# Optimization experiments

Hardware: AMD Instinct MI355X
Metric: run time of the kernel (lower is better)

The kernel has to match this reference:

```python
import jax, jax.numpy as jnp
import numpy as np

B, N, C = 8192, 4, 1024
H = 16
D = C // H              # head_dim = 64
P = 4                   # proj_dim (Linformer reduced length)
IDX_I, IDX_J = 1, 2     # Return_attn_way(use_cls=True, attn_selet_way=0)
SCALE = D ** -0.5


def setup_inputs() -> dict:
    key = jax.random.key(0)
    ks = jax.random.split(key, 6)
    std = 0.02
    x = jax.random.normal(ks[0], (B, N, C), dtype=jnp.float32)
    W_qkv = jax.random.normal(ks[1], (C, 3 * C), dtype=jnp.float32) * std   # qkv_bias=False
    W_proj = jax.random.normal(ks[2], (C, C), dtype=jnp.float32) * std
    b_proj = jnp.zeros((C,), dtype=jnp.float32)
    W_E = jax.random.normal(ks[3], (P, N), dtype=jnp.float32) * std         # torch Linear weight [out,in]
    W_F = jax.random.normal(ks[4], (P, N), dtype=jnp.float32) * std
    return {"x": x, "W_qkv": W_qkv, "W_proj": W_proj, "b_proj": b_proj,
            "W_E": W_E, "W_F": W_F}


def reference(x, W_qkv, W_proj, b_proj, W_E, W_F):
    b, n, c = x.shape
    # qkv projection -> [B,N,3,H,D] -> q,k,v each [B,H,N,D]
    qkv = (x @ W_qkv).reshape(b, n, 3, H, D)
    qkv = jnp.transpose(qkv, (2, 0, 3, 1, 4))
    q, k, v = qkv[0], qkv[1], qkv[2]
    q = q * SCALE  # q_norm/k_norm are Identity (qk_norm=False)

    # gathered single-token score: q[:,:,IDX_I,:] @ k[:,:,IDX_J,:].T -> [B,H,H]
    # (torch transpose(-2,-1) on the [B,H,D] slice swaps H and D)
    attn_sel = jnp.einsum('bhd,bgd->bhg', q[:, :, IDX_I, :], k[:, :, IDX_J, :])
    attn_sel_sig = jax.nn.sigmoid(attn_sel)

    # Linformer E/F projection along the sequence axis: [B,H,N,D] -> [B,H,P,D]
    k_low = jnp.einsum('bhnd,pn->bhpd', k, W_E)
    v_low = jnp.einsum('bhnd,pn->bhpd', v, W_F)

    # reduced softmax attention: [B,H,N,P]
    attn = jnp.einsum('bhnd,bhpd->bhnp', q, k_low)
    attn = jax.nn.softmax(attn, axis=-1)  # attn_drop is identity (p=0, eval)
    out = jnp.einsum('bhnp,bhpd->bhnd', attn, v_low)

    # merge heads and output projection
    out = jnp.transpose(out, (0, 2, 1, 3)).reshape(b, n, c)
    out = out @ W_proj.T + b_proj  # proj_drop identity
    return (out, attn_sel_sig)
```

## Files before the change

kernel.cpp:

```cpp
#include <hip/hip_runtime.h>
#include <hip/hip_bf16.h>

#define B_   8192
#define C_   1024
#define H_   16
#define M_   (B_ * 4)
#define K_   1024
#define N1_  3072

typedef __attribute__((ext_vector_type(8))) short short8;
typedef __attribute__((ext_vector_type(4))) float f32x4;
typedef __attribute__((ext_vector_type(8))) int   int8v;

__device__ __forceinline__ unsigned short f2bf(float f) {
  union { float f; unsigned u; } v; v.f = f;
  unsigned r = v.u + 0x7fffu + ((v.u >> 16) & 1u);
  return (unsigned short)(r >> 16);
}
__device__ __forceinline__ float bf2f(unsigned short u) {
  union { unsigned u; float f; } v; v.u = ((unsigned)u) << 16;
  return v.f;
}
__device__ __forceinline__ int pk_fp8(float a, float b, float c, float d) {
  int r = __builtin_amdgcn_cvt_pk_fp8_f32(a, b, 0, false);
  r = __builtin_amdgcn_cvt_pk_fp8_f32(c, d, r, true);
  return r;
}

__device__ __forceinline__ size_t bpack(int j, int c) {
  return (size_t)(j >> 4) * 16384 + (size_t)(c >> 7) * 2048 +
         (size_t)((c >> 4) & 1) * 1024 + (size_t)((c >> 5) & 3) * 256 +
         (size_t)(j & 15) * 16 + (size_t)(c & 15);
}

__global__ __launch_bounds__(256) void cast_x_k(const float* __restrict__ x,
                                                unsigned char* __restrict__ x8,
                                                unsigned short* __restrict__ xsel) {
  const int row = blockIdx.x;
  const int tid = threadIdx.x;
  float4 v = ((const float4*)(x + (size_t)row * 1024))[tid];
  ((int*)(x8 + (size_t)row * 1024))[tid] = pk_fp8(v.x, v.y, v.z, v.w);
  const int n = row & 3;
  if (n == 1 || n == 2) {
    ushort4 o;
    o.x = f2bf(v.x); o.y = f2bf(v.y); o.z = f2bf(v.z); o.w = f2bf(v.w);
    ((ushort4*)(xsel + ((size_t)(n - 1) * 8192 + (row >> 2)) * 1024))[tid] = o;
  }
}

__global__ __launch_bounds__(256) void transpose_wqkv_k(const float* __restrict__ in,
                                                        unsigned short* __restrict__ outb,
                                                        unsigned char* __restrict__ out8) {
  __shared__ float t[32][33];
  int tx = threadIdx.x, ty = threadIdx.y;
  int j0 = blockIdx.x * 32, c0 = blockIdx.y * 32;
#pragma unroll
  for (int i = 0; i < 4; ++i)
    t[ty + i * 8][tx] = in[(size_t)(c0 + ty + i * 8) * N1_ + j0 + tx];
  __syncthreads();
#pragma unroll
  for (int i = 0; i < 4; ++i) {
    int j = j0 + ty + i * 8;
    int c = c0 + tx;
    float v = t[tx][ty + i * 8];
    if (j < 1024) v *= 0.125f;
    outb[(size_t)j * K_ + c] = f2bf(v);
    out8[bpack(j, c)] =
        (unsigned char)(__builtin_amdgcn_cvt_pk_fp8_f32(v * 32.f, v * 32.f, 0, false) & 0xff);
  }
}

__global__ __launch_bounds__(256) void cast_wproj_k(const float* __restrict__ in,
                                                    unsigned char* __restrict__ out) {
  int i = blockIdx.x * 256 + threadIdx.x;
  float4 v = ((const float4*)in)[i];
  int f = i * 4;
  int j = f >> 10, c = f & 1023;
  *(int*)(out + bpack(j, c)) = pk_fp8(v.x * 32.f, v.y * 32.f, v.z * 32.f, v.w * 32.f);
}

__global__ __launch_bounds__(256) void gemm_fixup(const unsigned short* __restrict__ A,
                                                  const unsigned short* __restrict__ B0,
                                                  unsigned short* __restrict__ Cbf) {
  __shared__ unsigned short lsA[128 * 32];
  __shared__ unsigned short lsB[128 * 32];
  const int K = 1024, Ncols = 1024;
  const int tid = threadIdx.x;
  const int wave = tid >> 6, lane = tid & 63;
  const int wm = (wave >> 1) * 64, wn = (wave & 1) * 64;
  const long tile_m = (long)blockIdx.y * 128, tile_n = (long)blockIdx.x * 128;
  const unsigned short* Bm = B0 + (tile_m >= 8192 ? (size_t)1024 * 1024 : 0);

  f32x4 acc[4][4] = {};
  const int ci0 = (wave * 2 + 0) * 64 + lane;
  const int ci1 = (wave * 2 + 1) * 64 + lane;
  const int r0 = ci0 >> 2, kc0 = (ci0 & 3) * 8;
  const int r1 = ci1 >> 2, kc1 = (ci1 & 3) * 8;
  const unsigned short* gA0 = A + (tile_m + r0) * K + kc0;
  const unsigned short* gA1 = A + (tile_m + r1) * K + kc1;
  const unsigned short* gB0 = Bm + (tile_n + r0) * K + kc0;
  const unsigned short* gB1 = Bm + (tile_n + r1) * K + kc1;
  unsigned short* dA0 = lsA + (wave * 2 + 0) * 512;
  unsigned short* dA1 = lsA + (wave * 2 + 1) * 512;
  unsigned short* dB0 = lsB + (wave * 2 + 0) * 512;
  unsigned short* dB1 = lsB + (wave * 2 + 1) * 512;
  const int r16 = lane & 15, q8 = (lane >> 4) * 8;

  for (int kt = 0; kt < K; kt += 32) {
    __builtin_amdgcn_global_load_lds((const __attribute__((address_space(1))) void*)(gA0 + kt),
                                     (__attribute__((address_space(3))) void*)dA0, 16, 0, 0);
    __builtin_amdgcn_global_load_lds((const __attribute__((address_space(1))) void*)(gA1 + kt),
                                     (__attribute__((address_space(3))) void*)dA1, 16, 0, 0);
    __builtin_amdgcn_global_load_lds((const __attribute__((address_space(1))) void*)(gB0 + kt),
                                     (__attribute__((address_space(3))) void*)dB0, 16, 0, 0);
    __builtin_amdgcn_global_load_lds((const __attribute__((address_space(1))) void*)(gB1 + kt),
                                     (__attribute__((address_space(3))) void*)dB1, 16, 0, 0);
    __syncthreads();
    short8 afr[4], bfr[4];
#pragma unroll
    for (int mi = 0; mi < 4; ++mi)
      afr[mi] = *(const short8*)&lsA[(wm + mi * 16 + r16) * 32 + q8];
#pragma unroll
    for (int ni = 0; ni < 4; ++ni)
      bfr[ni] = *(const short8*)&lsB[(wn + ni * 16 + r16) * 32 + q8];
#pragma unroll
    for (int mi = 0; mi < 4; ++mi)
#pragma unroll
      for (int ni = 0; ni < 4; ++ni)
        acc[mi][ni] = __builtin_amdgcn_mfma_f32_16x16x32_bf16(afr[mi], bfr[ni], acc[mi][ni], 0, 0, 0);
    __syncthreads();
  }
  const int cl = lane & 15, rq = (lane >> 4) * 4;
#pragma unroll
  for (int mi = 0; mi < 4; ++mi)
#pragma unroll
    for (int ni = 0; ni < 4; ++ni) {
      long col = tile_n + wn + ni * 16 + cl;
#pragma unroll
      for (int r = 0; r < 4; ++r) {
        long row = tile_m + wm + mi * 16 + rq + r;
        Cbf[(size_t)row * Ncols + col] = f2bf(acc[mi][ni][r]);
      }
    }
}

template <int OUTMODE>
__global__ __launch_bounds__(256) void gemm_mx(const unsigned char* __restrict__ A,
                                               const unsigned char* __restrict__ Bm,
                                               unsigned short* __restrict__ Cbf,
                                               float* __restrict__ Cf,
                                               const float* __restrict__ bias,
                                               int Ncols, int sA, int sB) {
  __shared__ unsigned char lds[49152];

  const int tid = threadIdx.x;
  const int wave = tid >> 6, lane = tid & 63;
  const int wm = (wave >> 1) * 64, wn = (wave & 1) * 64;
  const int tile_m = blockIdx.y * 128, tile_n = blockIdx.x * 128;

  f32x4 acc[4][4] = {};

  unsigned offA[4];
#pragma unroll
  for (int j = 0; j < 4; ++j) {
    int ci = j * 256 + tid;
    int qgs = ci >> 8, id = ci & 255;
    int r2 = (id >> 3) & 1, r3 = (id >> 4) & 1;
    int rr0 = ((id >> 1) & 1) ^ r2, rr1 = ((id >> 2) & 1) ^ r3;
    int row = rr0 | (rr1 << 1) | (r2 << 2) | (r3 << 3) | ((id >> 5) << 4);
    int half = (id & 1) ^ rr0;
    offA[j] = (unsigned)((tile_m + row) * K_ + qgs * 32 + half * 16);
  }

  const int hl = lane & 15, qg = lane >> 4;
  const int swz = (hl & 12) << 3;
  const int laneFragBase = qg * 4096 + ((hl * 32) ^ swz) + ((hl & 1) << 4);

  const unsigned char* gB = Bm + (size_t)((tile_n + wn) >> 4) * 16384 + (size_t)lane * 16;

  auto stageA = [&](int t) {
    unsigned char* dA = lds + (t % 3) * 16384;
    const int kt = t << 7;
#pragma unroll
    for (int j = 0; j < 4; ++j)
      __builtin_amdgcn_global_load_lds(
          (const __attribute__((address_space(1))) void*)(A + offA[j] + kt),
          (__attribute__((address_space(3))) void*)(dA + (j * 256 + wave * 64) * 16), 16, 0, 0);
  };

  int8v b[4];
  auto loadB = [&](int t) {
    const int kt16 = t * 2048;
#pragma unroll
    for (int ni = 0; ni < 4; ++ni) {
      const unsigned char* bp = gB + (size_t)ni * 16384 + kt16;
      int4 h0 = *(const int4*)bp;
      int4 h1 = *(const int4*)(bp + 1024);
      b[ni] = int8v{h0.x, h0.y, h0.z, h0.w, h1.x, h1.y, h1.z, h1.w};
    }
  };

  stageA(0);
  stageA(1);
  loadB(0);

#pragma unroll
  for (int t = 0; t < 8; ++t) {
    if (t < 7) asm volatile("s_waitcnt vmcnt(12)" ::: "memory");
    else       asm volatile("s_waitcnt vmcnt(8)" ::: "memory");
    __builtin_amdgcn_s_barrier();
    if (t + 2 < 8) stageA(t + 2);

    unsigned char* bA = lds + (t % 3) * 16384;
    __builtin_amdgcn_s_setprio(1);
#pragma unroll
    for (int mi = 0; mi < 4; ++mi) {
      int ad = (wm + mi * 16) * 32 + laneFragBase;
      int4 h0 = *(const int4*)(bA + ad);
      int4 h1 = *(const int4*)(bA + (ad ^ 16));
      int8v af = int8v{h0.x, h0.y, h0.z, h0.w, h1.x, h1.y, h1.z, h1.w};
#pragma unroll
      for (int ni = 0; ni < 4; ++ni)
        acc[mi][ni] = __builtin_amdgcn_mfma_scale_f32_16x16x128_f8f6f4(
            af, b[ni], acc[mi][ni], 0, 0, 0, sA, 0, sB);
    }
    __builtin_amdgcn_s_setprio(0);

    if (t + 1 < 8) loadB(t + 1);
  }

  const int cl = lane & 15, rq = (lane >> 4) * 4;
#pragma unroll
  for (int mi = 0; mi < 4; ++mi)
#pragma unroll
    for (int ni = 0; ni < 4; ++ni) {
      long col = tile_n + wn + ni * 16 + cl;
      float bv = (OUTMODE == 1) ? bias[col] : 0.f;
#pragma unroll
      for (int r = 0; r < 4; ++r) {
        long row = tile_m + wm + mi * 16 + rq + r;
        if (OUTMODE == 0)
          Cbf[(size_t)row * Ncols + col] = f2bf(acc[mi][ni][r]);
        else
          Cf[(size_t)row * Ncols + col] = acc[mi][ni][r] + bv;
      }
    }
}

__global__ __launch_bounds__(256) void attn_mfma_k(const unsigned short* __restrict__ qkv,
                                                   const unsigned short* __restrict__ q1,
                                                   const unsigned short* __restrict__ k2,
                                                   const float* __restrict__ WE,
                                                   const float* __restrict__ WF,
                                                   unsigned char* __restrict__ hmid8,
                                                   float* __restrict__ attn_sel) {
  __shared__ float As[4][16 * 17 + 2];
  const int tid = threadIdx.x;
  const int wave = tid >> 6, lane = tid & 63;
  const int b = blockIdx.x * 4 + wave;
  const size_t qb = (size_t)b * 4 * N1_;
  const int hl = lane & 15, qg = lane >> 4;

  f32x4 accS[4][4] = {};
  f32x4 accSel = {};
#pragma unroll
  for (int ch = 0; ch < 2; ++ch) {
    const int off = ch * 32 + qg * 8;
    short8 qf[4], kf[4];
#pragma unroll
    for (int n = 0; n < 4; ++n)
      qf[n] = *(const short8*)(qkv + qb + (size_t)n * N1_ + 0 + hl * 64 + off);
#pragma unroll
    for (int m = 0; m < 4; ++m)
      kf[m] = *(const short8*)(qkv + qb + (size_t)m * N1_ + 1024 + hl * 64 + off);
#pragma unroll
    for (int n = 0; n < 4; ++n)
#pragma unroll
      for (int m = 0; m < 4; ++m)
        accS[n][m] = __builtin_amdgcn_mfma_f32_16x16x32_bf16(qf[n], kf[m], accS[n][m], 0, 0, 0);
    short8 qs = *(const short8*)(q1 + (size_t)b * 1024 + hl * 64 + off);
    short8 ks = *(const short8*)(k2 + (size_t)b * 1024 + hl * 64 + off);
    accSel = __builtin_amdgcn_mfma_f32_16x16x32_bf16(qs, ks, accSel, 0, 0, 0);
  }

#pragma unroll
  for (int r = 0; r < 4; ++r)
    attn_sel[(size_t)b * 256 + (qg * 4 + r) * 16 + hl] = 1.f / (1.f + __expf(-accSel[r]));

  if ((hl >> 2) == qg) {
    const int h = hl, rr = h & 3;
    float Sm[4][4];
#pragma unroll
    for (int n = 0; n < 4; ++n)
#pragma unroll
      for (int m = 0; m < 4; ++m) Sm[n][m] = accS[n][m][rr];
#pragma unroll
    for (int n = 0; n < 4; ++n) {
      float lg[4];
#pragma unroll
      for (int p = 0; p < 4; ++p)
        lg[p] = Sm[n][0] * WE[p * 4] + Sm[n][1] * WE[p * 4 + 1] +
                Sm[n][2] * WE[p * 4 + 2] + Sm[n][3] * WE[p * 4 + 3];
      float mx = fmaxf(fmaxf(lg[0], lg[1]), fmaxf(lg[2], lg[3]));
      float e0 = __expf(lg[0] - mx), e1 = __expf(lg[1] - mx);
      float e2 = __expf(lg[2] - mx), e3 = __expf(lg[3] - mx);
      float inv = 1.f / (e0 + e1 + e2 + e3);
      e0 *= inv; e1 *= inv; e2 *= inv; e3 *= inv;
#pragma unroll
      for (int m = 0; m < 4; ++m)
        As[wave][h * 17 + n * 4 + m] =
            e0 * WF[0 * 4 + m] + e1 * WF[1 * 4 + m] + e2 * WF[2 * 4 + m] + e3 * WF[3 * 4 + m];
    }
  }
  __syncthreads();

  {
    const int h = lane & 15, dg = lane >> 4;
    float Ap[4][4];
#pragma unroll
    for (int n = 0; n < 4; ++n)
#pragma unroll
      for (int m = 0; m < 4; ++m) Ap[n][m] = As[wave][h * 17 + n * 4 + m];

    float outv[4][16] = {};
#pragma unroll
    for (int m = 0; m < 4; ++m) {
      const unsigned short* vp = qkv + qb + (size_t)m * N1_ + 2048 + h * 64 + dg * 16;
      short8 v0 = *(const short8*)(vp);
      short8 v1 = *(const short8*)(vp + 8);
      float vf[16];
#pragma unroll
      for (int j = 0; j < 8; ++j) {
        vf[j] = bf2f((unsigned short)v0[j]);
        vf[8 + j] = bf2f((unsigned short)v1[j]);
      }
#pragma unroll
      for (int n = 0; n < 4; ++n)
#pragma unroll
        for (int d = 0; d < 16; ++d) outv[n][d] += Ap[n][m] * vf[d];
    }
#pragma unroll
    for (int n = 0; n < 4; ++n) {
      int w0 = pk_fp8(outv[n][0] * 32.f, outv[n][1] * 32.f, outv[n][2] * 32.f, outv[n][3] * 32.f);
      int w1 = pk_fp8(outv[n][4] * 32.f, outv[n][5] * 32.f, outv[n][6] * 32.f, outv[n][7] * 32.f);
      int w2 = pk_fp8(outv[n][8] * 32.f, outv[n][9] * 32.f, outv[n][10] * 32.f, outv[n][11] * 32.f);
      int w3 = pk_fp8(outv[n][12] * 32.f, outv[n][13] * 32.f, outv[n][14] * 32.f, outv[n][15] * 32.f);
      *(int4*)(hmid8 + ((size_t)b * 4 + n) * 1024 + h * 64 + dg * 16) = make_int4(w0, w1, w2, w3);
    }
  }
}

extern "C" void kernel_launch(void* const* d_in, const int* in_sizes, int n_in,
                              void* d_out, int out_size, void* d_ws, size_t ws_size,
                              hipStream_t stream) {
  (void)in_sizes; (void)n_in; (void)out_size; (void)ws_size;
  const float* x      = (const float*)d_in[0];
  const float* W_qkv  = (const float*)d_in[1];
  const float* W_proj = (const float*)d_in[2];
  const float* b_proj = (const float*)d_in[3];
  const float* W_E    = (const float*)d_in[4];
  const float* W_F    = (const float*)d_in[5];

  float* out0 = (float*)d_out;
  float* out1 = out0 + (size_t)M_ * C_;

  char* ws = (char*)d_ws;
  unsigned short* xsel   = (unsigned short*)(ws);
  unsigned short* wqkvTb = (unsigned short*)(ws + 33554432);
  unsigned short* qkv_bf = (unsigned short*)(ws);
  unsigned char*  x8     = (unsigned char*)(ws + 201326592);
  unsigned char*  hmid8  = x8;
  unsigned char*  wqkvT8 = (unsigned char*)(ws + 234881024);
  unsigned char*  wproj8 = (unsigned char*)(ws + 238026752);
  unsigned short* q1k2   = (unsigned short*)(ws + 239075328);

  cast_x_k<<<32768, 256, 0, stream>>>(x, x8, xsel);
  transpose_wqkv_k<<<dim3(96, 32), dim3(32, 8), 0, stream>>>(W_qkv, wqkvTb, wqkvT8);
  cast_wproj_k<<<1024, 256, 0, stream>>>(W_proj, wproj8);

  gemm_fixup<<<dim3(8, 128), 256, 0, stream>>>(xsel, wqkvTb, q1k2);

  gemm_mx<0><<<dim3(24, 256), 256, 0, stream>>>(x8, wqkvT8, qkv_bf, nullptr, nullptr,
                                                3072, 127, 122);

  attn_mfma_k<<<B_ / 4, 256, 0, stream>>>(qkv_bf, q1k2, q1k2 + (size_t)8192 * 1024,
                                          W_E, W_F, hmid8, out1);

  gemm_mx<1><<<dim3(8, 256), 256, 0, stream>>>(hmid8, wproj8, nullptr, out0, b_proj,
                                               1024, 122, 122);
}
```

Measured before the change: 546.7 us.

## Pre-pack A operands into MFMA fragment layout and drop LDS staging

The x cast kernel and the attention kernel now write their fp8 outputs directly in the pre-swizzled fragment layout already used for the B operand. The fp8 GEMM can then load A fragments straight from global memory into registers, with double-buffered register prefetch replacing the three-stage LDS pipeline and its barriers. This removes LDS traffic and synchronisation. In exchange, each wave loads its A fragments itself with no sharing through LDS, which raises global and L2 traffic and register pressure.

```diff
diff --git a/kernel.cpp b/kernel.cpp
--- a/kernel.cpp
+++ b/kernel.cpp
@@ -36,15 +36,41 @@
 __global__ __launch_bounds__(256) void cast_x_k(const float* __restrict__ x,
                                                 unsigned char* __restrict__ x8,
                                                 unsigned short* __restrict__ xsel) {
-  const int row = blockIdx.x;
-  const int tid = threadIdx.x;
-  float4 v = ((const float4*)(x + (size_t)row * 1024))[tid];
-  ((int*)(x8 + (size_t)row * 1024))[tid] = pk_fp8(v.x, v.y, v.z, v.w);
+  const int rg = blockIdx.x;
+  const int t = threadIdx.x;
+  const int hl = t >> 4;
+  const int ck = t & 15;
+  const int row = rg * 16 + hl;
   const int n = row & 3;
-  if (n == 1 || n == 2) {
-    ushort4 o;
-    o.x = f2bf(v.x); o.y = f2bf(v.y); o.z = f2bf(v.z); o.w = f2bf(v.w);
-    ((ushort4*)(xsel + ((size_t)(n - 1) * 8192 + (row >> 2)) * 1024))[tid] = o;
+  const float* xr = x + (size_t)row * 1024;
+  unsigned char* og = x8 + (size_t)rg * 16384 + hl * 16;
+  unsigned short* xr2 = (n == 1 || n == 2)
+      ? xsel + ((size_t)(n - 1) * 8192 + (row >> 2)) * 1024 : nullptr;
+#pragma unroll
+  for (int i = 0; i < 4; ++i) {
+    const int kk = ck + i * 16;
+    const int c = kk * 16;
+    float4 v0 = *(const float4*)(xr + c);
+    float4 v1 = *(const float4*)(xr + c + 4);
+    float4 v2 = *(const float4*)(xr + c + 8);
+    float4 v3 = *(const float4*)(xr + c + 12);
+    int4 o;
+    o.x = pk_fp8(v0.x, v0.y, v0.z, v0.w);
+    o.y = pk_fp8(v1.x, v1.y, v1.z, v1.w);
+    o.z = pk_fp8(v2.x, v2.y, v2.z, v2.w);
+    o.w = pk_fp8(v3.x, v3.y, v3.z, v3.w);
+    *(int4*)(og + (kk >> 3) * 2048 + (kk & 1) * 1024 + ((kk >> 1) & 3) * 256) = o;
+    if (xr2) {
+      ushort4 s0, s1, s2, s3;
+      s0.x = f2bf(v0.x); s0.y = f2bf(v0.y); s0.z = f2bf(v0.z); s0.w = f2bf(v0.w);
+      s1.x = f2bf(v1.x); s1.y = f2bf(v1.y); s1.z = f2bf(v1.z); s1.w = f2bf(v1.w);
+      s2.x = f2bf(v2.x); s2.y = f2bf(v2.y); s2.z = f2bf(v2.z); s2.w = f2bf(v2.w);
+      s3.x = f2bf(v3.x); s3.y = f2bf(v3.y); s3.z = f2bf(v3.z); s3.w = f2bf(v3.w);
+      *(ushort4*)(xr2 + c) = s0;
+      *(ushort4*)(xr2 + c + 4) = s1;
+      *(ushort4*)(xr2 + c + 8) = s2;
+      *(ushort4*)(xr2 + c + 12) = s3;
+    }
   }
 }
 
@@ -151,82 +177,45 @@
                                                float* __restrict__ Cf,
                                                const float* __restrict__ bias,
                                                int Ncols, int sA, int sB) {
-  __shared__ unsigned char lds[49152];
-
   const int tid = threadIdx.x;
   const int wave = tid >> 6, lane = tid & 63;
   const int wm = (wave >> 1) * 64, wn = (wave & 1) * 64;
   const int tile_m = blockIdx.y * 128, tile_n = blockIdx.x * 128;
 
   f32x4 acc[4][4] = {};
-
-  unsigned offA[4];
-#pragma unroll
-  for (int j = 0; j < 4; ++j) {
-    int ci = j * 256 + tid;
-    int qgs = ci >> 8, id = ci & 255;
-    int r2 = (id >> 3) & 1, r3 = (id >> 4) & 1;
-    int rr0 = ((id >> 1) & 1) ^ r2, rr1 = ((id >> 2) & 1) ^ r3;
-    int row = rr0 | (rr1 << 1) | (r2 << 2) | (r3 << 3) | ((id >> 5) << 4);
-    int half = (id & 1) ^ rr0;
-    offA[j] = (unsigned)((tile_m + row) * K_ + qgs * 32 + half * 16);
-  }
-
-  const int hl = lane & 15, qg = lane >> 4;
-  const int swz = (hl & 12) << 3;
-  const int laneFragBase = qg * 4096 + ((hl * 32) ^ swz) + ((hl & 1) << 4);
-
+  const unsigned char* gA = A + (size_t)((tile_m + wm) >> 4) * 16384 + (size_t)lane * 16;
   const unsigned char* gB = Bm + (size_t)((tile_n + wn) >> 4) * 16384 + (size_t)lane * 16;
 
-  auto stageA = [&](int t) {
-    unsigned char* dA = lds + (t % 3) * 16384;
-    const int kt = t << 7;
-#pragma unroll
-    for (int j = 0; j < 4; ++j)
-      __builtin_amdgcn_global_load_lds(
-          (const __attribute__((address_space(1))) void*)(A + offA[j] + kt),
-          (__attribute__((address_space(3))) void*)(dA + (j * 256 + wave * 64) * 16), 16, 0, 0);
+  int8v aP[4], bP[4], aQ[4], bQ[4];
+
+  auto load8 = [&](const unsigned char* g, int t, int8v* dst) {
+    const int kt16 = t * 2048;
+#pragma unroll
+    for (int i = 0; i < 4; ++i) {
+      const unsigned char* p = g + (size_t)i * 16384 + kt16;
+      int4 h0 = *(const int4*)p;
+      int4 h1 = *(const int4*)(p + 1024);
+      dst[i] = int8v{h0.x, h0.y, h0.z, h0.w, h1.x, h1.y, h1.z, h1.w};
+    }
   };
 
-  int8v b[4];
-  auto loadB = [&](int t) {
-    const int kt16 = t * 2048;
-#pragma unroll
-    for (int ni = 0; ni < 4; ++ni) {
-      const unsigned char* bp = gB + (size_t)ni * 16384 + kt16;
-      int4 h0 = *(const int4*)bp;
-      int4 h1 = *(const int4*)(bp + 1024);
-      b[ni] = int8v{h0.x, h0.y, h0.z, h0.w, h1.x, h1.y, h1.z, h1.w};
-    }
-  };
-
-  stageA(0);
-  stageA(1);
-  loadB(0);
-
+  load8(gA, 0, aP);
+  load8(gB, 0, bP);
 #pragma unroll
   for (int t = 0; t < 8; ++t) {
-    if (t < 7) asm volatile("s_waitcnt vmcnt(12)" ::: "memory");
-    else       asm volatile("s_waitcnt vmcnt(8)" ::: "memory");
-    __builtin_amdgcn_s_barrier();
-    if (t + 2 < 8) stageA(t + 2);
-
-    unsigned char* bA = lds + (t % 3) * 16384;
+    const int8v* ca = (t & 1) ? aQ : aP;
+    const int8v* cb = (t & 1) ? bQ : bP;
+    int8v* na = (t & 1) ? aP : aQ;
+    int8v* nb = (t & 1) ? bP : bQ;
+    if (t + 1 < 8) { load8(gA, t + 1, na); load8(gB, t + 1, nb); }
     __builtin_amdgcn_s_setprio(1);
 #pragma unroll
-    for (int mi = 0; mi < 4; ++mi) {
-      int ad = (wm + mi * 16) * 32 + laneFragBase;
-      int4 h0 = *(const int4*)(bA + ad);
-      int4 h1 = *(const int4*)(bA + (ad ^ 16));
-      int8v af = int8v{h0.x, h0.y, h0.z, h0.w, h1.x, h1.y, h1.z, h1.w};
+    for (int mi = 0; mi < 4; ++mi)
 #pragma unroll
       for (int ni = 0; ni < 4; ++ni)
         acc[mi][ni] = __builtin_amdgcn_mfma_scale_f32_16x16x128_f8f6f4(
-            af, b[ni], acc[mi][ni], 0, 0, 0, sA, 0, sB);
-    }
+            ca[mi], cb[ni], acc[mi][ni], 0, 0, 0, sA, 0, sB);
     __builtin_amdgcn_s_setprio(0);
-
-    if (t + 1 < 8) loadB(t + 1);
   }
 
   const int cl = lane & 15, rq = (lane >> 4) * 4;
@@ -345,7 +334,7 @@
       int w1 = pk_fp8(outv[n][4] * 32.f, outv[n][5] * 32.f, outv[n][6] * 32.f, outv[n][7] * 32.f);
       int w2 = pk_fp8(outv[n][8] * 32.f, outv[n][9] * 32.f, outv[n][10] * 32.f, outv[n][11] * 32.f);
       int w3 = pk_fp8(outv[n][12] * 32.f, outv[n][13] * 32.f, outv[n][14] * 32.f, outv[n][15] * 32.f);
-      *(int4*)(hmid8 + ((size_t)b * 4 + n) * 1024 + h * 64 + dg * 16) = make_int4(w0, w1, w2, w3);
+      *(int4*)(hmid8 + bpack(b * 4 + n, h * 64 + dg * 16)) = make_int4(w0, w1, w2, w3);
     }
   }
 }
@@ -374,7 +363,7 @@
   unsigned char*  wproj8 = (unsigned char*)(ws + 238026752);
   unsigned short* q1k2   = (unsigned short*)(ws + 239075328);
 
-  cast_x_k<<<32768, 256, 0, stream>>>(x, x8, xsel);
+  cast_x_k<<<2048, 256, 0, stream>>>(x, x8, xsel);
   transpose_wqkv_k<<<dim3(96, 32), dim3(32, 8), 0, stream>>>(W_qkv, wqkvTb, wqkvT8);
   cast_wproj_k<<<1024, 256, 0, stream>>>(W_proj, wproj8);
 
```

New measurement: 566.9 us. +3.7%, slower.
